# Kernel optimization log

Hardware: AMD Instinct MI355X
Metric: run time of the kernel (lower is better)

Reference implementation:

```python
import jax, jax.numpy as jnp
import numpy as np

EPS = 1e-5  # torch LayerNorm default


def _ln(x, g, b):
    m = jnp.mean(x, axis=-1, keepdims=True)
    v = jnp.mean((x - m) ** 2, axis=-1, keepdims=True)
    return (x - m) / jnp.sqrt(v + EPS) * g + b


def setup_inputs() -> dict:
    key = jax.random.key(0)
    ks = jax.random.split(key, 16)
    B, C, H, S, FF, BINS = 2048, 20, 256, 64, 512, 128
    f32 = jnp.float32
    def w(k, shape, s=0.02):
        return jax.random.normal(k, shape, f32) * s
    return {
        "bitplanes": jax.random.normal(ks[0], (B, C, 8, 8), f32),
        "conv1_w": w(ks[1], (H, C, 3, 3), 0.05), "conv1_b": jnp.zeros((H,), f32),
        "conv2_w": w(ks[2], (H, H, 3, 3), 0.05), "conv2_b": jnp.zeros((H,), f32),
        "in_proj_w": w(ks[3], (3 * H, H)), "in_proj_b": jnp.zeros((3 * H,), f32),
        "out_proj_w": w(ks[4], (H, H)), "out_proj_b": jnp.zeros((H,), f32),
        "ln1_g": jnp.ones((H,), f32), "ln1_b": jnp.zeros((H,), f32),
        "ff1_w": w(ks[5], (FF, H)), "ff1_b": jnp.zeros((FF,), f32),
        "ff2_w": w(ks[6], (H, FF)), "ff2_b": jnp.zeros((H,), f32),
        "ln2_g": jnp.ones((H,), f32), "ln2_b": jnp.zeros((H,), f32),
        "be1_w": w(ks[7], (H, H * S)), "be1_b": jnp.zeros((H,), f32),
        "be2_w": w(ks[8], (H, H)), "be2_b": jnp.zeros((H,), f32),
        "L1_w": w(ks[9], (H, 3 * H)), "L1_b": jnp.zeros((H,), f32),
        "L2_w": w(ks[10], (H, H)), "L2_b": jnp.zeros((H,), f32),
        "Lln_g": jnp.ones((H,), f32), "Lln_b": jnp.zeros((H,), f32),
        "H1_w": w(ks[11], (H, 2 * H)), "H1_b": jnp.zeros((H,), f32),
        "H2_w": w(ks[12], (H, H)), "H2_b": jnp.zeros((H,), f32),
        "Hln_g": jnp.ones((H,), f32), "Hln_b": jnp.zeros((H,), f32),
        "v1_w": w(ks[13], (H, H)), "v1_b": jnp.zeros((H,), f32),
        "v2_w": w(ks[14], (BINS, H)), "v2_b": jnp.zeros((BINS,), f32),
    }


def reference(bitplanes, conv1_w, conv1_b, conv2_w, conv2_b,
              in_proj_w, in_proj_b, out_proj_w, out_proj_b,
              ln1_g, ln1_b, ff1_w, ff1_b, ff2_w, ff2_b, ln2_g, ln2_b,
              be1_w, be1_b, be2_w, be2_b,
              L1_w, L1_b, L2_w, L2_b, Lln_g, Lln_b,
              H1_w, H1_b, H2_w, H2_b, Hln_g, Hln_b,
              v1_w, v1_b, v2_w, v2_b):
    N, T, Hd, nh = 8, 8, 256, 4
    B = bitplanes.shape[0]
    dn = ('NCHW', 'OIHW', 'NCHW')
    # conv encoder on 8x8 board
    x = jax.nn.relu(jax.lax.conv_general_dilated(bitplanes, conv1_w, (1, 1), 'SAME', dimension_numbers=dn) + conv1_b[None, :, None, None])
    x = jax.nn.relu(jax.lax.conv_general_dilated(x, conv2_w, (1, 1), 'SAME', dimension_numbers=dn) + conv2_b[None, :, None, None])
    x = x.reshape(B, Hd, 64).transpose(0, 2, 1)  # [B, 64, 256]
    # TransformerEncoderLayer (post-norm, eval mode => dropout off)
    qkv = x @ in_proj_w.T + in_proj_b  # [B, 64, 768]
    q, k, v = jnp.split(qkv, 3, axis=-1)
    dh = Hd // nh
    heads = lambda t: t.reshape(B, 64, nh, dh).transpose(0, 2, 1, 3)
    q, k, v = heads(q), heads(k), heads(v)
    scale = 1.0 / float(dh) ** 0.5
    a = jax.nn.softmax(jnp.einsum('bhqd,bhkd->bhqk', q, k) * scale, axis=-1)
    o = jnp.einsum('bhqk,bhkd->bhqd', a, v).transpose(0, 2, 1, 3).reshape(B, 64, Hd)
    o = o @ out_proj_w.T + out_proj_b
    x = _ln(x + o, ln1_g, ln1_b)
    ff = jax.nn.relu(x @ ff1_w.T + ff1_b) @ ff2_w.T + ff2_b
    x = _ln(x + ff, ln2_g, ln2_b)
    xf = x.reshape(B, 64 * Hd)  # [B, 16384]
    be = jax.nn.relu(jax.nn.relu(xf @ be1_w.T + be1_b) @ be2_w.T + be2_b)

    def Lnet(zL, zH):
        h = jax.nn.relu(jnp.concatenate([zL, zH, be], axis=-1) @ L1_w.T + L1_b)
        return _ln(jax.nn.relu(h @ L2_w.T + L2_b), Lln_g, Lln_b)

    def Hnet(zH, zL):
        h = jax.nn.relu(jnp.concatenate([zH, zL], axis=-1) @ H1_w.T + H1_b)
        return _ln(jax.nn.relu(h @ H2_w.T + H2_b), Hln_g, Hln_b)

    z0 = jnp.zeros((B, Hd), x.dtype)

    def step(carry, i):
        zH, zL = carry
        zL = Lnet(zL, zH)
        zH = jnp.where((i + 1) % T == 0, Hnet(zH, zL), zH)  # H update every T steps
        return (zH, zL), None

    (zH, zL), _ = jax.lax.scan(step, (z0, z0), jnp.arange(N * T - 1))
    zL = Lnet(zL, zH)
    zH = Hnet(zH, zL)
    return jax.nn.relu(zH @ v1_w.T + v1_b) @ v2_w.T + v2_b  # [B, 128]
```

## Files before the change

kernel.cpp:

```cpp
#include <hip/hip_runtime.h>
#include <hip/hip_bf16.h>
#include <math.h>

#define DEV __device__ __forceinline__

typedef __attribute__((ext_vector_type(8))) short s16x8;
typedef __attribute__((ext_vector_type(4))) float f32x4;

DEV f32x4 MF(s16x8 a, s16x8 b, f32x4 c) {
    return __builtin_amdgcn_mfma_f32_16x16x32_bf16(a, b, c, 0, 0, 0);
}

DEV void split8store(const float v[8], unsigned short* d) {
    s16x8 vh, vm, vl;
#pragma unroll
    for (int j = 0; j < 8; ++j) {
        const float x = v[j];
        const unsigned u = __float_as_uint(x);
        vh[j] = (short)(u >> 16);
        const float r1 = x - __uint_as_float(u & 0xffff0000u);
        const unsigned u1 = __float_as_uint(r1);
        vm[j] = (short)(u1 >> 16);
        const float r2 = r1 - __uint_as_float(u1 & 0xffff0000u);
        vl[j] = (short)(__float_as_uint(r2) >> 16);
    }
    *(s16x8*)(d) = vh;
    *(s16x8*)(d + 512) = vm;
    *(s16x8*)(d + 1024) = vl;
}

__global__ void k_tpose(const float* __restrict__ in, float* __restrict__ out, int N, int K) {
    int total = N * K;
    for (int idx = blockIdx.x * blockDim.x + threadIdx.x; idx < total; idx += gridDim.x * blockDim.x) {
        int n = idx / K, k = idx - n * K;
        out[k * N + n] = in[idx];
    }
}

__global__ void k_wpack(const float* __restrict__ W, unsigned short* __restrict__ WP, int K) {
    const int idx = blockIdx.x * 256 + threadIdx.x;
    const int total = (K >> 5) * 16 * 64;
    if (idx >= total) return;
    const int lane = idx & 63;
    const int nt = (idx >> 6) & 15;
    const int ks = idx >> 10;
    const int col = nt * 16 + (lane & 15);
    const int k0 = ks * 32 + ((lane >> 4) << 3);
    const float* src = W + (size_t)col * K + k0;
    const float4 p = *(const float4*)src;
    const float4 q = *(const float4*)(src + 4);
    const float v[8] = {p.x, p.y, p.z, p.w, q.x, q.y, q.z, q.w};
    split8store(v, WP + (size_t)((ks * 16 + nt) * 3) * 512 + lane * 8);
}

__global__ __launch_bounds__(256) void k_conv1(const float* __restrict__ in, const float* __restrict__ w,
                                               const float* __restrict__ bias, float* __restrict__ out) {
    __shared__ __align__(16) float img[20 * 100];
    const int b = blockIdx.x;
    const int t = threadIdx.x;
    for (int idx = t; idx < 2000; idx += 256) {
        int c = idx / 100, pp = idx - c * 100;
        int y = pp / 10, x = pp - y * 10;
        float v = 0.f;
        if (y >= 1 && y <= 8 && x >= 1 && x <= 8)
            v = in[((size_t)b * 20 + c) * 64 + (y - 1) * 8 + (x - 1)];
        img[idx] = v;
    }
    __syncthreads();
    const int oc = t;
    float acc[64];
    const float bz = bias[oc];
#pragma unroll
    for (int p = 0; p < 64; ++p) acc[p] = bz;
    const float* wrow = w + oc * 180;
    for (int c = 0; c < 20; ++c) {
#pragma unroll
        for (int k = 0; k < 9; ++k) {
            const int ky = k / 3, kx = k - ky * 3;
            const float wv = wrow[c * 9 + k];
            const int base = c * 100 + ky * 10 + kx;
#pragma unroll
            for (int p = 0; p < 64; ++p)
                acc[p] = fmaf(wv, img[base + p + ((p >> 3) << 1)], acc[p]);
        }
    }
    float* orow = out + ((size_t)b * 256 + oc) * 64;
#pragma unroll
    for (int p = 0; p < 64; ++p) orow[p] = fmaxf(acc[p], 0.f);
}

__global__ __launch_bounds__(256) void k_conv2(const float* __restrict__ a1, const float* __restrict__ w2t,
                                               const float* __restrict__ bias, float* __restrict__ xout) {
    __shared__ __align__(16) float img[128 * 100];
    const int b = blockIdx.x;
    const int t = threadIdx.x;
    const int oc0 = (t & 63) * 4;
    const int pg = t >> 6;
    const int pos0 = pg * 16;
    float acc[4][16];
#pragma unroll
    for (int i = 0; i < 4; ++i) {
        const float bz = bias[oc0 + i];
#pragma unroll
        for (int j = 0; j < 16; ++j) acc[i][j] = bz;
    }
    for (int half = 0; half < 2; ++half) {
        __syncthreads();
        for (int idx = t; idx < 12800; idx += 256) {
            int c = idx / 100, pp = idx - c * 100;
            int y = pp / 10, x = pp - y * 10;
            float v = 0.f;
            if (y >= 1 && y <= 8 && x >= 1 && x <= 8)
                v = a1[((size_t)b * 256 + half * 128 + c) * 64 + (y - 1) * 8 + (x - 1)];
            img[idx] = v;
        }
        __syncthreads();
        for (int ic = 0; ic < 128; ++ic) {
            const float* wbase = w2t + (size_t)((half * 128 + ic) * 9) * 256 + oc0;
#pragma unroll
            for (int k = 0; k < 9; ++k) {
                const int ky = k / 3, kx = k - ky * 3;
                const float4 w4 = *(const float4*)(wbase + k * 256);
                const int rb = ic * 100 + ky * 10 + kx + pg * 20;
#pragma unroll
                for (int j = 0; j < 16; ++j) {
                    const float v = img[rb + j + ((j >> 3) << 1)];
                    acc[0][j] = fmaf(v, w4.x, acc[0][j]);
                    acc[1][j] = fmaf(v, w4.y, acc[1][j]);
                    acc[2][j] = fmaf(v, w4.z, acc[2][j]);
                    acc[3][j] = fmaf(v, w4.w, acc[3][j]);
                }
            }
        }
    }
#pragma unroll
    for (int j = 0; j < 16; ++j) {
        float4 o4 = make_float4(fmaxf(acc[0][j], 0.f), fmaxf(acc[1][j], 0.f),
                                fmaxf(acc[2][j], 0.f), fmaxf(acc[3][j], 0.f));
        *(float4*)(xout + ((size_t)b * 64 + pos0 + j) * 256 + oc0) = o4;
    }
}

__global__ __launch_bounds__(512) void k_attn(const float* __restrict__ x, const float* __restrict__ wqkvT,
                                              const float* __restrict__ bqkv, float* __restrict__ o) {
    __shared__ __align__(16) float qs[64 * 65];
    __shared__ __align__(16) float ks[64 * 68];
    __shared__ __align__(16) float vs[64 * 68];
    __shared__ float pmax[8 * 64];
    __shared__ float psum[8 * 64];
    const int b = blockIdx.x, h = blockIdx.y;
    const int t = threadIdx.x;
    const int d = t & 63;
    const int pg = t >> 6;
    float aq[8], ak[8], av[8];
#pragma unroll
    for (int j = 0; j < 8; ++j) { aq[j] = 0.f; ak[j] = 0.f; av[j] = 0.f; }
    const float* xrow = x + ((size_t)b * 64 + pg * 8) * 256;
    const int colq = h * 64 + d;
    for (int kk = 0; kk < 256; kk += 4) {
        float wq[4], wk[4], wv[4];
#pragma unroll
        for (int i = 0; i < 4; ++i) {
            const float* wr = wqkvT + (size_t)(kk + i) * 768;
            wq[i] = wr[colq]; wk[i] = wr[256 + colq]; wv[i] = wr[512 + colq];
        }
#pragma unroll
        for (int j = 0; j < 8; ++j) {
            const float4 xv = *(const float4*)(xrow + j * 256 + kk);
            aq[j] = fmaf(xv.x, wq[0], aq[j]); aq[j] = fmaf(xv.y, wq[1], aq[j]);
            aq[j] = fmaf(xv.z, wq[2], aq[j]); aq[j] = fmaf(xv.w, wq[3], aq[j]);
            ak[j] = fmaf(xv.x, wk[0], ak[j]); ak[j] = fmaf(xv.y, wk[1], ak[j]);
            ak[j] = fmaf(xv.z, wk[2], ak[j]); ak[j] = fmaf(xv.w, wk[3], ak[j]);
            av[j] = fmaf(xv.x, wv[0], av[j]); av[j] = fmaf(xv.y, wv[1], av[j]);
            av[j] = fmaf(xv.z, wv[2], av[j]); av[j] = fmaf(xv.w, wv[3], av[j]);
        }
    }
    const float bq = bqkv[colq], bk = bqkv[256 + colq], bv = bqkv[512 + colq];
#pragma unroll
    for (int j = 0; j < 8; ++j) {
        const int p = pg * 8 + j;
        qs[p * 65 + d] = aq[j] + bq;
        ks[p * 68 + d] = ak[j] + bk;
        vs[p * 68 + d] = av[j] + bv;
    }
    __syncthreads();
    const int r = t & 63;
    const int cg = t >> 6;
    float sc[8];
#pragma unroll
    for (int j = 0; j < 8; ++j) sc[j] = 0.f;
    for (int kk = 0; kk < 64; kk += 4) {
        float qv[4];
#pragma unroll
        for (int i = 0; i < 4; ++i) qv[i] = qs[r * 65 + kk + i];
#pragma unroll
        for (int j = 0; j < 8; ++j) {
            const float4 kv = *(const float4*)(ks + (cg * 8 + j) * 68 + kk);
            sc[j] = fmaf(qv[0], kv.x, sc[j]); sc[j] = fmaf(qv[1], kv.y, sc[j]);
            sc[j] = fmaf(qv[2], kv.z, sc[j]); sc[j] = fmaf(qv[3], kv.w, sc[j]);
        }
    }
    float pm = -1e30f;
#pragma unroll
    for (int j = 0; j < 8; ++j) { sc[j] *= 0.125f; pm = fmaxf(pm, sc[j]); }
    pmax[cg * 64 + r] = pm;
    __syncthreads();
    float m = pmax[r];
#pragma unroll
    for (int i = 1; i < 8; ++i) m = fmaxf(m, pmax[i * 64 + r]);
    float pe[8], ps = 0.f;
#pragma unroll
    for (int j = 0; j < 8; ++j) { pe[j] = __expf(sc[j] - m); ps += pe[j]; }
    psum[cg * 64 + r] = ps;
    __syncthreads();
    float den = psum[r];
#pragma unroll
    for (int i = 1; i < 8; ++i) den += psum[i * 64 + r];
    const float rden = 1.f / den;
#pragma unroll
    for (int j = 0; j < 8; ++j) qs[r * 65 + cg * 8 + j] = pe[j] * rden;
    __syncthreads();
    float oa[8];
#pragma unroll
    for (int j = 0; j < 8; ++j) oa[j] = 0.f;
    for (int c = 0; c < 64; ++c) {
        const float pv = qs[r * 65 + c];
        const float4 v0 = *(const float4*)(vs + c * 68 + cg * 8);
        const float4 v1 = *(const float4*)(vs + c * 68 + cg * 8 + 4);
        oa[0] = fmaf(pv, v0.x, oa[0]); oa[1] = fmaf(pv, v0.y, oa[1]);
        oa[2] = fmaf(pv, v0.z, oa[2]); oa[3] = fmaf(pv, v0.w, oa[3]);
        oa[4] = fmaf(pv, v1.x, oa[4]); oa[5] = fmaf(pv, v1.y, oa[5]);
        oa[6] = fmaf(pv, v1.z, oa[6]); oa[7] = fmaf(pv, v1.w, oa[7]);
    }
#pragma unroll
    for (int j = 0; j < 8; ++j) ks[r * 68 + cg * 8 + j] = oa[j];
    __syncthreads();
    for (int idx = t; idx < 4096; idx += 512) {
        const int rr = idx >> 6, dd = idx & 63;
        o[((size_t)b * 64 + rr) * 256 + h * 64 + dd] = ks[rr * 68 + dd];
    }
}

__global__ __launch_bounds__(256) void k_gemm(const float* __restrict__ A, const float* __restrict__ W,
                                              const float* __restrict__ bias, float* __restrict__ C,
                                              int M, int N, int K, int kChunk, int relu) {
    __shared__ __align__(16) float As[16 * 68];
    __shared__ __align__(16) float Bs[16 * 68];
    const int t = threadIdx.x;
    const int row0 = blockIdx.x * 64;
    const int col0 = blockIdx.y * 64;
    const int k0 = blockIdx.z * kChunk;
    const int k1 = k0 + kChunk;
    float* Cb = C + (size_t)blockIdx.z * M * N;
    const int tr = t >> 4, tc = t & 15;
    const int lr = t >> 2, lc = t & 3;
    float acc[4][4] = {};
    const float* Ap = A + (size_t)(row0 + lr) * K + lc * 4;
    const float* Wp = W + (size_t)(col0 + lr) * K + lc * 4;
    for (int kt = k0; kt < k1; kt += 16) {
        const float4 a4 = *(const float4*)(Ap + kt);
        const float4 w4 = *(const float4*)(Wp + kt);
        As[(lc * 4 + 0) * 68 + lr] = a4.x;
        As[(lc * 4 + 1) * 68 + lr] = a4.y;
        As[(lc * 4 + 2) * 68 + lr] = a4.z;
        As[(lc * 4 + 3) * 68 + lr] = a4.w;
        Bs[(lc * 4 + 0) * 68 + lr] = w4.x;
        Bs[(lc * 4 + 1) * 68 + lr] = w4.y;
        Bs[(lc * 4 + 2) * 68 + lr] = w4.z;
        Bs[(lc * 4 + 3) * 68 + lr] = w4.w;
        __syncthreads();
#pragma unroll
        for (int kk = 0; kk < 16; ++kk) {
            const float4 av = *(const float4*)(As + kk * 68 + tr * 4);
            const float4 bv = *(const float4*)(Bs + kk * 68 + tc * 4);
            acc[0][0] = fmaf(av.x, bv.x, acc[0][0]); acc[0][1] = fmaf(av.x, bv.y, acc[0][1]);
            acc[0][2] = fmaf(av.x, bv.z, acc[0][2]); acc[0][3] = fmaf(av.x, bv.w, acc[0][3]);
            acc[1][0] = fmaf(av.y, bv.x, acc[1][0]); acc[1][1] = fmaf(av.y, bv.y, acc[1][1]);
            acc[1][2] = fmaf(av.y, bv.z, acc[1][2]); acc[1][3] = fmaf(av.y, bv.w, acc[1][3]);
            acc[2][0] = fmaf(av.z, bv.x, acc[2][0]); acc[2][1] = fmaf(av.z, bv.y, acc[2][1]);
            acc[2][2] = fmaf(av.z, bv.z, acc[2][2]); acc[2][3] = fmaf(av.z, bv.w, acc[2][3]);
            acc[3][0] = fmaf(av.w, bv.x, acc[3][0]); acc[3][1] = fmaf(av.w, bv.y, acc[3][1]);
            acc[3][2] = fmaf(av.w, bv.z, acc[3][2]); acc[3][3] = fmaf(av.w, bv.w, acc[3][3]);
        }
        __syncthreads();
    }
    float4 bb = make_float4(0.f, 0.f, 0.f, 0.f);
    if (bias) bb = *(const float4*)(bias + col0 + tc * 4);
#pragma unroll
    for (int i = 0; i < 4; ++i) {
        float4 ov = make_float4(acc[i][0] + bb.x, acc[i][1] + bb.y, acc[i][2] + bb.z, acc[i][3] + bb.w);
        if (relu) {
            ov.x = fmaxf(ov.x, 0.f); ov.y = fmaxf(ov.y, 0.f);
            ov.z = fmaxf(ov.z, 0.f); ov.w = fmaxf(ov.w, 0.f);
        }
        *(float4*)(Cb + (size_t)(row0 + tr * 4 + i) * N + col0 + tc * 4) = ov;
    }
}

__global__ __launch_bounds__(256) void k_ln_add(float* __restrict__ x, const float* __restrict__ add,
                                                const float* __restrict__ g, const float* __restrict__ bta) {
    const int t = threadIdx.x;
    const size_t r = (size_t)blockIdx.x * 4 + (t >> 6);
    const int lane = t & 63;
    float4 xv = *(const float4*)(x + r * 256 + lane * 4);
    const float4 av = *(const float4*)(add + r * 256 + lane * 4);
    const float4 v = make_float4(xv.x + av.x, xv.y + av.y, xv.z + av.z, xv.w + av.w);
    float s = v.x + v.y + v.z + v.w;
    float ss = fmaf(v.x, v.x, fmaf(v.y, v.y, fmaf(v.z, v.z, v.w * v.w)));
#pragma unroll
    for (int m = 32; m; m >>= 1) { s += __shfl_xor(s, m); ss += __shfl_xor(ss, m); }
    const float mean = s * (1.f / 256.f);
    const float var = ss * (1.f / 256.f) - mean * mean;
    const float rstd = rsqrtf(var + 1e-5f);
    const float4 g4 = *(const float4*)(g + lane * 4);
    const float4 b4 = *(const float4*)(bta + lane * 4);
    float4 ov;
    ov.x = (v.x - mean) * rstd * g4.x + b4.x;
    ov.y = (v.y - mean) * rstd * g4.y + b4.y;
    ov.z = (v.z - mean) * rstd * g4.z + b4.z;
    ov.w = (v.w - mean) * rstd * g4.w + b4.w;
    *(float4*)(x + r * 256 + lane * 4) = ov;
}

__global__ void k_be1_reduce(const float* __restrict__ parts, const float* __restrict__ bias,
                             float* __restrict__ out, int n) {
    const int idx = blockIdx.x * blockDim.x + threadIdx.x;
    if (idx < n) {
        float s = bias[idx & 255];
#pragma unroll
        for (int p = 0; p < 8; ++p) s += parts[(size_t)p * n + idx];
        out[idx] = fmaxf(s, 0.f);
    }
}


DEV void splitpass(const float* scr, unsigned short* frag, int t) {
    const int ks = t >> 6, ln = t & 63;
    const int row = ln & 15;
    const int k0 = ks * 32 + ((ln >> 4) << 3);
    const float* s = scr + row * 260 + k0;
    const float4 p = *(const float4*)s;
    const float4 q = *(const float4*)(s + 4);
    const float v[8] = {p.x, p.y, p.z, p.w, q.x, q.y, q.z, q.w};
    split8store(v, frag + (ks * 3) * 512 + ln * 8);
}

DEV void mfma6(f32x4& acc, s16x8 ah, s16x8 am, s16x8 al, const unsigned short* bp) {
    const s16x8 bh = *(const s16x8*)(bp);
    const s16x8 bm = *(const s16x8*)(bp + 512);
    const s16x8 bl = *(const s16x8*)(bp + 1024);
    acc = MF(ah, bh, acc);
    acc = MF(ah, bm, acc);
    acc = MF(am, bh, acc);
    acc = MF(ah, bl, acc);
    acc = MF(al, bh, acc);
    acc = MF(am, bm, acc);
}

DEV void rungemm(f32x4& a0, f32x4& a1, const unsigned short* __restrict__ WP, int KS,
                 const unsigned short* f0, const unsigned short* f1, const unsigned short* f2,
                 int wv, int lane) {
    for (int ks = 0; ks < KS; ++ks) {
        const unsigned short* fa = (ks < 8) ? f0 : ((ks < 16) ? f1 : f2);
        const int kl = ks & 7;
        const unsigned short* ap = fa + (kl * 3) * 512 + lane * 8;
        const s16x8 ah = *(const s16x8*)(ap);
        const s16x8 am = *(const s16x8*)(ap + 512);
        const s16x8 al = *(const s16x8*)(ap + 1024);
        const unsigned short* bp = WP + (size_t)((ks * 16 + wv * 2) * 3) * 512 + lane * 8;
        mfma6(a0, ah, am, al, bp);
        mfma6(a1, ah, am, al, bp + 1536);
    }
}

DEV void storeC(f32x4 a0, f32x4 a1, const float* __restrict__ bias, float* scr, int wv, int lane) {
    const int rb = (lane >> 4) * 4;
    const int c0 = wv * 32 + (lane & 15);
    const float bz0 = bias[c0];
    const float bz1 = bias[c0 + 16];
    scr[(rb + 0) * 260 + c0] = fmaxf(a0[0] + bz0, 0.f);
    scr[(rb + 1) * 260 + c0] = fmaxf(a0[1] + bz0, 0.f);
    scr[(rb + 2) * 260 + c0] = fmaxf(a0[2] + bz0, 0.f);
    scr[(rb + 3) * 260 + c0] = fmaxf(a0[3] + bz0, 0.f);
    scr[(rb + 0) * 260 + c0 + 16] = fmaxf(a1[0] + bz1, 0.f);
    scr[(rb + 1) * 260 + c0 + 16] = fmaxf(a1[1] + bz1, 0.f);
    scr[(rb + 2) * 260 + c0 + 16] = fmaxf(a1[2] + bz1, 0.f);
    scr[(rb + 3) * 260 + c0 + 16] = fmaxf(a1[3] + bz1, 0.f);
}

DEV void lnpass(float* scr, const float* __restrict__ g, const float* __restrict__ bb, int t) {
    const int row = 2 * (t >> 6) + ((t & 63) >> 5);
    const int c0 = (t & 31) * 8;
    float* s = scr + row * 260 + c0;
    const float4 x0 = *(const float4*)s;
    const float4 x1 = *(const float4*)(s + 4);
    float sum = x0.x + x0.y + x0.z + x0.w + x1.x + x1.y + x1.z + x1.w;
    float sq = fmaf(x0.x, x0.x, fmaf(x0.y, x0.y, fmaf(x0.z, x0.z, x0.w * x0.w)));
    sq = fmaf(x1.x, x1.x, fmaf(x1.y, x1.y, fmaf(x1.z, x1.z, fmaf(x1.w, x1.w, sq))));
#pragma unroll
    for (int m = 16; m; m >>= 1) { sum += __shfl_xor(sum, m); sq += __shfl_xor(sq, m); }
    const float mean = sum * (1.f / 256.f);
    const float var = sq * (1.f / 256.f) - mean * mean;
    const float rstd = rsqrtf(var + 1e-5f);
    const float4 g0 = *(const float4*)(g + c0);
    const float4 g1 = *(const float4*)(g + c0 + 4);
    const float4 b0 = *(const float4*)(bb + c0);
    const float4 b1 = *(const float4*)(bb + c0 + 4);
    float4 o0, o1;
    o0.x = (x0.x - mean) * rstd * g0.x + b0.x;
    o0.y = (x0.y - mean) * rstd * g0.y + b0.y;
    o0.z = (x0.z - mean) * rstd * g0.z + b0.z;
    o0.w = (x0.w - mean) * rstd * g0.w + b0.w;
    o1.x = (x1.x - mean) * rstd * g1.x + b1.x;
    o1.y = (x1.y - mean) * rstd * g1.y + b1.y;
    o1.z = (x1.z - mean) * rstd * g1.z + b1.z;
    o1.w = (x1.w - mean) * rstd * g1.w + b1.w;
    *(float4*)s = o0;
    *(float4*)(s + 4) = o1;
}

__global__ __launch_bounds__(512, 1) void k_hrm(const float* __restrict__ be,
        const unsigned short* __restrict__ L1P, const float* __restrict__ L1b,
        const unsigned short* __restrict__ L2P, const float* __restrict__ L2b,
        const float* __restrict__ Lg, const float* __restrict__ Lbt,
        const unsigned short* __restrict__ H1P, const float* __restrict__ H1b,
        const unsigned short* __restrict__ H2P, const float* __restrict__ H2b,
        const float* __restrict__ Hg, const float* __restrict__ Hbt,
        const unsigned short* __restrict__ v1P, const float* __restrict__ v1b,
        const float* __restrict__ v2T, const float* __restrict__ v2b,
        float* __restrict__ out) {
    __shared__ __align__(16) unsigned short fzL[12288];
    __shared__ __align__(16) unsigned short fzH[12288];
    __shared__ __align__(16) unsigned short fbe[12288];
    __shared__ __align__(16) unsigned short fh1[12288];
    __shared__ __align__(16) float scr[16 * 260];
    const int t = threadIdx.x;
    const int b0 = blockIdx.x * 16;
    const int wv = t >> 6, lane = t & 63;
    for (int i = t; i < 12288; i += 512) { fzL[i] = 0; fzH[i] = 0; }
    {
        const int ks = t >> 6, ln = t & 63;
        const int row = ln & 15;
        const int k0 = ks * 32 + ((ln >> 4) << 3);
        const float* s = be + (size_t)(b0 + row) * 256 + k0;
        const float4 p = *(const float4*)s;
        const float4 q = *(const float4*)(s + 4);
        const float v[8] = {p.x, p.y, p.z, p.w, q.x, q.y, q.z, q.w};
        split8store(v, fbe + (ks * 3) * 512 + ln * 8);
    }
    __syncthreads();
    const f32x4 zero4 = {0.f, 0.f, 0.f, 0.f};
    for (int it = 0; it < 64; ++it) {
        f32x4 a0 = zero4, a1 = zero4;
        rungemm(a0, a1, L1P, 24, fzL, fzH, fbe, wv, lane);
        storeC(a0, a1, L1b, scr, wv, lane);
        __syncthreads();
        splitpass(scr, fh1, t);
        __syncthreads();
        a0 = zero4; a1 = zero4;
        rungemm(a0, a1, L2P, 8, fh1, fh1, fh1, wv, lane);
        storeC(a0, a1, L2b, scr, wv, lane);
        __syncthreads();
        lnpass(scr, Lg, Lbt, t);
        __syncthreads();
        splitpass(scr, fzL, t);
        __syncthreads();
        if (((it + 1) & 7) == 0) {
            a0 = zero4; a1 = zero4;
            rungemm(a0, a1, H1P, 16, fzH, fzL, fzL, wv, lane);
            storeC(a0, a1, H1b, scr, wv, lane);
            __syncthreads();
            splitpass(scr, fh1, t);
            __syncthreads();
            a0 = zero4; a1 = zero4;
            rungemm(a0, a1, H2P, 8, fh1, fh1, fh1, wv, lane);
            storeC(a0, a1, H2b, scr, wv, lane);
            __syncthreads();
            lnpass(scr, Hg, Hbt, t);
            __syncthreads();
            splitpass(scr, fzH, t);
            __syncthreads();
        }
    }
    f32x4 a0 = zero4, a1 = zero4;
    rungemm(a0, a1, v1P, 8, fzH, fzH, fzH, wv, lane);
    storeC(a0, a1, v1b, scr, wv, lane);
    __syncthreads();
    for (int idx = t; idx < 2048; idx += 512) {
        const int r = idx >> 7, oo = idx & 127;
        float s = v2b[oo];
        for (int kk = 0; kk < 256; kk += 4) {
            const float4 c4 = *(const float4*)(&scr[r * 260 + kk]);
            s = fmaf(c4.x, v2T[(kk + 0) * 128 + oo], s);
            s = fmaf(c4.y, v2T[(kk + 1) * 128 + oo], s);
            s = fmaf(c4.z, v2T[(kk + 2) * 128 + oo], s);
            s = fmaf(c4.w, v2T[(kk + 3) * 128 + oo], s);
        }
        out[(size_t)(b0 + r) * 128 + oo] = s;
    }
}

extern "C" void kernel_launch(void* const* d_in, const int* in_sizes, int n_in,
                              void* d_out, int out_size, void* d_ws, size_t ws_size,
                              hipStream_t stream) {
    const float* bitplanes  = (const float*)d_in[0];
    const float* conv1_w    = (const float*)d_in[1];
    const float* conv1_b    = (const float*)d_in[2];
    const float* conv2_w    = (const float*)d_in[3];
    const float* conv2_b    = (const float*)d_in[4];
    const float* in_proj_w  = (const float*)d_in[5];
    const float* in_proj_b  = (const float*)d_in[6];
    const float* out_proj_w = (const float*)d_in[7];
    const float* out_proj_b = (const float*)d_in[8];
    const float* ln1_g      = (const float*)d_in[9];
    const float* ln1_b      = (const float*)d_in[10];
    const float* ff1_w      = (const float*)d_in[11];
    const float* ff1_b      = (const float*)d_in[12];
    const float* ff2_w      = (const float*)d_in[13];
    const float* ff2_b      = (const float*)d_in[14];
    const float* ln2_g      = (const float*)d_in[15];
    const float* ln2_b      = (const float*)d_in[16];
    const float* be1_w      = (const float*)d_in[17];
    const float* be1_b      = (const float*)d_in[18];
    const float* be2_w      = (const float*)d_in[19];
    const float* be2_b      = (const float*)d_in[20];
    const float* L1_w       = (const float*)d_in[21];
    const float* L1_b       = (const float*)d_in[22];
    const float* L2_w       = (const float*)d_in[23];
    const float* L2_b       = (const float*)d_in[24];
    const float* Lln_g      = (const float*)d_in[25];
    const float* Lln_b      = (const float*)d_in[26];
    const float* H1_w       = (const float*)d_in[27];
    const float* H1_b       = (const float*)d_in[28];
    const float* H2_w       = (const float*)d_in[29];
    const float* H2_b       = (const float*)d_in[30];
    const float* Hln_g      = (const float*)d_in[31];
    const float* Hln_b      = (const float*)d_in[32];
    const float* v1_w       = (const float*)d_in[33];
    const float* v1_b       = (const float*)d_in[34];
    const float* v2_w       = (const float*)d_in[35];
    const float* v2_b       = (const float*)d_in[36];

    const size_t persist = 2654208ull;
    int CB = 64;
    for (int c = 2048; c >= 64; c >>= 1) {
        size_t needBytes = ((size_t)c * 65536ull + persist) * 4ull;
        if (needBytes <= ws_size) { CB = c; break; }
    }
    const int NCH = 2048 / CB;

    float* ws = (float*)d_ws;
    float* a1buf = ws;
    float* xbuf  = a1buf + (size_t)CB * 16384;
    float* tbuf  = xbuf + (size_t)CB * 16384;
    float* wqkvT = tbuf + (size_t)CB * 32768;
    float* w2t   = wqkvT + 196608;
    float* v2T   = w2t + 589824;
    float* L1Pf  = v2T + 32768;
    float* L2Pf  = L1Pf + 294912;
    float* H1Pf  = L2Pf + 98304;
    float* H2Pf  = H1Pf + 196608;
    float* v1Pf  = H2Pf + 98304;
    float* beB   = v1Pf + 98304;
    float* bemid = beB + 524288;
    unsigned short* L1P = (unsigned short*)L1Pf;
    unsigned short* L2P = (unsigned short*)L2Pf;
    unsigned short* H1P = (unsigned short*)H1Pf;
    unsigned short* H2P = (unsigned short*)H2Pf;
    unsigned short* v1P = (unsigned short*)v1Pf;

    k_tpose<<<256, 256, 0, stream>>>(in_proj_w, wqkvT, 768, 256);
    k_tpose<<<512, 256, 0, stream>>>(conv2_w, w2t, 256, 2304);
    k_tpose<<<64, 256, 0, stream>>>(v2_w, v2T, 128, 256);
    k_wpack<<<96, 256, 0, stream>>>(L1_w, L1P, 768);
    k_wpack<<<32, 256, 0, stream>>>(L2_w, L2P, 256);
    k_wpack<<<64, 256, 0, stream>>>(H1_w, H1P, 512);
    k_wpack<<<32, 256, 0, stream>>>(H2_w, H2P, 256);
    k_wpack<<<32, 256, 0, stream>>>(v1_w, v1P, 256);

    for (int ch = 0; ch < NCH; ++ch) {
        const float* bp_c = bitplanes + (size_t)ch * CB * 20 * 64;
        k_conv1<<<CB, 256, 0, stream>>>(bp_c, conv1_w, conv1_b, a1buf);
        k_conv2<<<CB, 256, 0, stream>>>(a1buf, w2t, conv2_b, xbuf);
        k_attn<<<dim3(CB, 4), 512, 0, stream>>>(xbuf, wqkvT, in_proj_b, a1buf);
        k_gemm<<<dim3(CB, 4, 1), 256, 0, stream>>>(a1buf, out_proj_w, out_proj_b, tbuf,
                                                   CB * 64, 256, 256, 256, 0);
        k_ln_add<<<CB * 16, 256, 0, stream>>>(xbuf, tbuf, ln1_g, ln1_b);
        k_gemm<<<dim3(CB, 8, 1), 256, 0, stream>>>(xbuf, ff1_w, ff1_b, tbuf,
                                                   CB * 64, 512, 256, 256, 1);
        k_gemm<<<dim3(CB, 4, 1), 256, 0, stream>>>(tbuf, ff2_w, ff2_b, a1buf,
                                                   CB * 64, 256, 512, 512, 0);
        k_ln_add<<<CB * 16, 256, 0, stream>>>(xbuf, a1buf, ln2_g, ln2_b);
        k_gemm<<<dim3(CB / 64, 4, 8), 256, 0, stream>>>(xbuf, be1_w, nullptr, tbuf,
                                                        CB, 256, 16384, 2048, 0);
        k_be1_reduce<<<CB, 256, 0, stream>>>(tbuf, be1_b, bemid + (size_t)ch * CB * 256, CB * 256);
        k_gemm<<<dim3(CB / 64, 4, 1), 256, 0, stream>>>(bemid + (size_t)ch * CB * 256, be2_w, be2_b,
                                                        beB + (size_t)ch * CB * 256, CB, 256, 256, 256, 1);
    }

    k_hrm<<<128, 512, 0, stream>>>(beB, L1P, L1_b, L2P, L2_b, Lln_g, Lln_b,
                                   H1P, H1_b, H2P, H2_b, Hln_g, Hln_b,
                                   v1P, v1_b, v2T, v2_b, (float*)d_out);
}
```

Before: 6.144 ms.

## Move conv2 and dense GEMMs to split-bf16 MFMA with prepacked weights

```diff
diff --git a/kernel.cpp b/kernel.cpp
--- a/kernel.cpp
+++ b/kernel.cpp
@@ -11,18 +11,23 @@
     return __builtin_amdgcn_mfma_f32_16x16x32_bf16(a, b, c, 0, 0, 0);
 }
 
+DEV void split3(float x, unsigned short& h, unsigned short& m, unsigned short& l) {
+    const unsigned u = __float_as_uint(x);
+    h = (unsigned short)(u >> 16);
+    const float r1 = x - __uint_as_float(u & 0xffff0000u);
+    const unsigned u1 = __float_as_uint(r1);
+    m = (unsigned short)(u1 >> 16);
+    const float r2 = r1 - __uint_as_float(u1 & 0xffff0000u);
+    l = (unsigned short)(__float_as_uint(r2) >> 16);
+}
+
 DEV void split8store(const float v[8], unsigned short* d) {
     s16x8 vh, vm, vl;
 #pragma unroll
     for (int j = 0; j < 8; ++j) {
-        const float x = v[j];
-        const unsigned u = __float_as_uint(x);
-        vh[j] = (short)(u >> 16);
-        const float r1 = x - __uint_as_float(u & 0xffff0000u);
-        const unsigned u1 = __float_as_uint(r1);
-        vm[j] = (short)(u1 >> 16);
-        const float r2 = r1 - __uint_as_float(u1 & 0xffff0000u);
-        vl[j] = (short)(__float_as_uint(r2) >> 16);
+        unsigned short h, m, l;
+        split3(v[j], h, m, l);
+        vh[j] = (short)h; vm[j] = (short)m; vl[j] = (short)l;
     }
     *(s16x8*)(d) = vh;
     *(s16x8*)(d + 512) = vm;
@@ -37,25 +42,27 @@
     }
 }
 
-__global__ void k_wpack(const float* __restrict__ W, unsigned short* __restrict__ WP, int K) {
+__global__ void k_wpack3(const float* __restrict__ W, unsigned short* __restrict__ WP,
+                         int K, int NT, int ldw, int stride, int off) {
     const int idx = blockIdx.x * 256 + threadIdx.x;
-    const int total = (K >> 5) * 16 * 64;
+    const int total = (K >> 5) * NT * 64;
     if (idx >= total) return;
     const int lane = idx & 63;
-    const int nt = (idx >> 6) & 15;
-    const int ks = idx >> 10;
+    const int nt = (idx >> 6) % NT;
+    const int ks = idx / (64 * NT);
     const int col = nt * 16 + (lane & 15);
     const int k0 = ks * 32 + ((lane >> 4) << 3);
-    const float* src = W + (size_t)col * K + k0;
-    const float4 p = *(const float4*)src;
-    const float4 q = *(const float4*)(src + 4);
-    const float v[8] = {p.x, p.y, p.z, p.w, q.x, q.y, q.z, q.w};
-    split8store(v, WP + (size_t)((ks * 16 + nt) * 3) * 512 + lane * 8);
+    const float* src = W + (size_t)col * ldw + (size_t)k0 * stride + off;
+    float v[8];
+#pragma unroll
+    for (int j = 0; j < 8; ++j) v[j] = src[j * stride];
+    split8store(v, WP + (size_t)((ks * NT + nt) * 3) * 512 + lane * 8);
 }
 
 __global__ __launch_bounds__(256) void k_conv1(const float* __restrict__ in, const float* __restrict__ w,
                                                const float* __restrict__ bias, float* __restrict__ out) {
     __shared__ __align__(16) float img[20 * 100];
+    __shared__ __align__(16) float stg[16 * 260];
     const int b = blockIdx.x;
     const int t = threadIdx.x;
     for (int idx = t; idx < 2000; idx += 256) {
@@ -84,65 +91,93 @@
                 acc[p] = fmaf(wv, img[base + p + ((p >> 3) << 1)], acc[p]);
         }
     }
-    float* orow = out + ((size_t)b * 256 + oc) * 64;
-#pragma unroll
-    for (int p = 0; p < 64; ++p) orow[p] = fmaxf(acc[p], 0.f);
-}
-
-__global__ __launch_bounds__(256) void k_conv2(const float* __restrict__ a1, const float* __restrict__ w2t,
-                                               const float* __restrict__ bias, float* __restrict__ xout) {
-    __shared__ __align__(16) float img[128 * 100];
-    const int b = blockIdx.x;
-    const int t = threadIdx.x;
-    const int oc0 = (t & 63) * 4;
-    const int pg = t >> 6;
-    const int pos0 = pg * 16;
-    float acc[4][16];
-#pragma unroll
-    for (int i = 0; i < 4; ++i) {
-        const float bz = bias[oc0 + i];
-#pragma unroll
-        for (int j = 0; j < 16; ++j) acc[i][j] = bz;
-    }
-    for (int half = 0; half < 2; ++half) {
+#pragma unroll
+    for (int cc = 0; cc < 4; ++cc) {
+        __syncthreads();
+#pragma unroll
+        for (int p = 0; p < 16; ++p) stg[p * 260 + t] = acc[cc * 16 + p];
+        __syncthreads();
+        for (int idx = t; idx < 4096; idx += 256) {
+            const int r = idx >> 8, c = idx & 255;
+            out[((size_t)b * 64 + cc * 16 + r) * 256 + c] = fmaxf(stg[r * 260 + c], 0.f);
+        }
+    }
+}
+
+__global__ __launch_bounds__(256) void k_conv2mf(const float* __restrict__ a1,
+                                                 const unsigned short* __restrict__ WPC2,
+                                                 const float* __restrict__ bias,
+                                                 float* __restrict__ xout) {
+    __shared__ __align__(16) unsigned short AhS[100 * 132];
+    __shared__ __align__(16) unsigned short AmS[100 * 132];
+    __shared__ __align__(16) unsigned short AlS[100 * 132];
+    const int b = blockIdx.x, t = threadIdx.x;
+    const int wv = t >> 6, lane = t & 63;
+    f32x4 acc[16];
+#pragma unroll
+    for (int nt = 0; nt < 16; ++nt) acc[nt] = (f32x4){0.f, 0.f, 0.f, 0.f};
+    const int pl = lane & 15;
+    const int py = pl >> 3, px = pl & 7;
+    const int akoff = (lane >> 4) << 3;
+    for (int h = 0; h < 2; ++h) {
         __syncthreads();
         for (int idx = t; idx < 12800; idx += 256) {
-            int c = idx / 100, pp = idx - c * 100;
-            int y = pp / 10, x = pp - y * 10;
+            const int pr = idx >> 7, c = idx & 127;
+            const int Y = pr / 10, X = pr - Y * 10;
             float v = 0.f;
-            if (y >= 1 && y <= 8 && x >= 1 && x <= 8)
-                v = a1[((size_t)b * 256 + half * 128 + c) * 64 + (y - 1) * 8 + (x - 1)];
-            img[idx] = v;
-        }
-        __syncthreads();
-        for (int ic = 0; ic < 128; ++ic) {
-            const float* wbase = w2t + (size_t)((half * 128 + ic) * 9) * 256 + oc0;
-#pragma unroll
-            for (int k = 0; k < 9; ++k) {
-                const int ky = k / 3, kx = k - ky * 3;
-                const float4 w4 = *(const float4*)(wbase + k * 256);
-                const int rb = ic * 100 + ky * 10 + kx + pg * 20;
-#pragma unroll
-                for (int j = 0; j < 16; ++j) {
-                    const float v = img[rb + j + ((j >> 3) << 1)];
-                    acc[0][j] = fmaf(v, w4.x, acc[0][j]);
-                    acc[1][j] = fmaf(v, w4.y, acc[1][j]);
-                    acc[2][j] = fmaf(v, w4.z, acc[2][j]);
-                    acc[3][j] = fmaf(v, w4.w, acc[3][j]);
+            if (Y >= 1 && Y <= 8 && X >= 1 && X <= 8)
+                v = a1[((size_t)b * 64 + (Y - 1) * 8 + X - 1) * 256 + h * 128 + c];
+            unsigned short hh, mm, ll;
+            split3(v, hh, mm, ll);
+            AhS[pr * 132 + c] = hh;
+            AmS[pr * 132 + c] = mm;
+            AlS[pr * 132 + c] = ll;
+        }
+        __syncthreads();
+#pragma unroll
+        for (int tap = 0; tap < 9; ++tap) {
+            const int dy = tap / 3, dx = tap - dy * 3;
+            const int prow = (wv * 2 + py + dy) * 10 + px + dx;
+            const unsigned short* arh = AhS + prow * 132 + akoff;
+            const unsigned short* arm = AmS + prow * 132 + akoff;
+            const unsigned short* arl = AlS + prow * 132 + akoff;
+#pragma unroll
+            for (int ks = 0; ks < 4; ++ks) {
+                const s16x8 ah = *(const s16x8*)(arh + ks * 32);
+                const s16x8 am = *(const s16x8*)(arm + ks * 32);
+                const s16x8 al = *(const s16x8*)(arl + ks * 32);
+                const unsigned short* bp = WPC2 + (size_t)(tap * 128 + (h * 4 + ks) * 16) * 1536 + lane * 8;
+#pragma unroll
+                for (int nt = 0; nt < 16; ++nt) {
+                    const unsigned short* bb = bp + nt * 1536;
+                    const s16x8 bh = *(const s16x8*)(bb);
+                    const s16x8 bm = *(const s16x8*)(bb + 512);
+                    const s16x8 bl = *(const s16x8*)(bb + 1024);
+                    acc[nt] = MF(ah, bh, acc[nt]);
+                    acc[nt] = MF(ah, bm, acc[nt]);
+                    acc[nt] = MF(am, bh, acc[nt]);
+                    acc[nt] = MF(ah, bl, acc[nt]);
+                    acc[nt] = MF(al, bh, acc[nt]);
+                    acc[nt] = MF(am, bm, acc[nt]);
                 }
             }
         }
     }
-#pragma unroll
-    for (int j = 0; j < 16; ++j) {
-        float4 o4 = make_float4(fmaxf(acc[0][j], 0.f), fmaxf(acc[1][j], 0.f),
-                                fmaxf(acc[2][j], 0.f), fmaxf(acc[3][j], 0.f));
-        *(float4*)(xout + ((size_t)b * 64 + pos0 + j) * 256 + oc0) = o4;
+    const int prow0 = wv * 16 + ((lane >> 4) << 2);
+    const int ccol = lane & 15;
+#pragma unroll
+    for (int nt = 0; nt < 16; ++nt) {
+        const float bz = bias[nt * 16 + ccol];
+#pragma unroll
+        for (int i = 0; i < 4; ++i)
+            xout[((size_t)b * 64 + prow0 + i) * 256 + nt * 16 + ccol] = fmaxf(acc[nt][i] + bz, 0.f);
     }
 }
 
 __global__ __launch_bounds__(512) void k_attn(const float* __restrict__ x, const float* __restrict__ wqkvT,
-                                              const float* __restrict__ bqkv, float* __restrict__ o) {
+                                              const float* __restrict__ bqkv,
+                                              unsigned short* __restrict__ oh, unsigned short* __restrict__ om,
+                                              unsigned short* __restrict__ ol) {
     __shared__ __align__(16) float qs[64 * 65];
     __shared__ __align__(16) float ks[64 * 68];
     __shared__ __align__(16) float vs[64 * 68];
@@ -237,68 +272,98 @@
     __syncthreads();
     for (int idx = t; idx < 4096; idx += 512) {
         const int rr = idx >> 6, dd = idx & 63;
-        o[((size_t)b * 64 + rr) * 256 + h * 64 + dd] = ks[rr * 68 + dd];
-    }
-}
-
-__global__ __launch_bounds__(256) void k_gemm(const float* __restrict__ A, const float* __restrict__ W,
-                                              const float* __restrict__ bias, float* __restrict__ C,
-                                              int M, int N, int K, int kChunk, int relu) {
-    __shared__ __align__(16) float As[16 * 68];
-    __shared__ __align__(16) float Bs[16 * 68];
+        const float v = ks[rr * 68 + dd];
+        unsigned short hh, mm, ll;
+        split3(v, hh, mm, ll);
+        const size_t o = ((size_t)b * 64 + rr) * 256 + h * 64 + dd;
+        oh[o] = hh;
+        om[o] = mm;
+        ol[o] = ll;
+    }
+}
+
+__global__ __launch_bounds__(256) void k_gemm_mf(
+    const unsigned short* __restrict__ Ah, const unsigned short* __restrict__ Am,
+    const unsigned short* __restrict__ Al,
+    const unsigned short* __restrict__ WP, const float* __restrict__ bias,
+    float* __restrict__ Cf, unsigned short* __restrict__ Ch, unsigned short* __restrict__ Cm,
+    unsigned short* __restrict__ Cl,
+    int M, int N, int K, int kChunk, int relu) {
     const int t = threadIdx.x;
-    const int row0 = blockIdx.x * 64;
+    const int wv = t >> 6, lane = t & 63;
+    const int row0 = blockIdx.x * 64 + wv * 16;
     const int col0 = blockIdx.y * 64;
+    const int NT = N >> 4;
     const int k0 = blockIdx.z * kChunk;
-    const int k1 = k0 + kChunk;
-    float* Cb = C + (size_t)blockIdx.z * M * N;
-    const int tr = t >> 4, tc = t & 15;
-    const int lr = t >> 2, lc = t & 3;
-    float acc[4][4] = {};
-    const float* Ap = A + (size_t)(row0 + lr) * K + lc * 4;
-    const float* Wp = W + (size_t)(col0 + lr) * K + lc * 4;
-    for (int kt = k0; kt < k1; kt += 16) {
-        const float4 a4 = *(const float4*)(Ap + kt);
-        const float4 w4 = *(const float4*)(Wp + kt);
-        As[(lc * 4 + 0) * 68 + lr] = a4.x;
-        As[(lc * 4 + 1) * 68 + lr] = a4.y;
-        As[(lc * 4 + 2) * 68 + lr] = a4.z;
-        As[(lc * 4 + 3) * 68 + lr] = a4.w;
-        Bs[(lc * 4 + 0) * 68 + lr] = w4.x;
-        Bs[(lc * 4 + 1) * 68 + lr] = w4.y;
-        Bs[(lc * 4 + 2) * 68 + lr] = w4.z;
-        Bs[(lc * 4 + 3) * 68 + lr] = w4.w;
-        __syncthreads();
-#pragma unroll
-        for (int kk = 0; kk < 16; ++kk) {
-            const float4 av = *(const float4*)(As + kk * 68 + tr * 4);
-            const float4 bv = *(const float4*)(Bs + kk * 68 + tc * 4);
-            acc[0][0] = fmaf(av.x, bv.x, acc[0][0]); acc[0][1] = fmaf(av.x, bv.y, acc[0][1]);
-            acc[0][2] = fmaf(av.x, bv.z, acc[0][2]); acc[0][3] = fmaf(av.x, bv.w, acc[0][3]);
-            acc[1][0] = fmaf(av.y, bv.x, acc[1][0]); acc[1][1] = fmaf(av.y, bv.y, acc[1][1]);
-            acc[1][2] = fmaf(av.y, bv.z, acc[1][2]); acc[1][3] = fmaf(av.y, bv.w, acc[1][3]);
-            acc[2][0] = fmaf(av.z, bv.x, acc[2][0]); acc[2][1] = fmaf(av.z, bv.y, acc[2][1]);
-            acc[2][2] = fmaf(av.z, bv.z, acc[2][2]); acc[2][3] = fmaf(av.z, bv.w, acc[2][3]);
-            acc[3][0] = fmaf(av.w, bv.x, acc[3][0]); acc[3][1] = fmaf(av.w, bv.y, acc[3][1]);
-            acc[3][2] = fmaf(av.w, bv.z, acc[3][2]); acc[3][3] = fmaf(av.w, bv.w, acc[3][3]);
-        }
-        __syncthreads();
-    }
-    float4 bb = make_float4(0.f, 0.f, 0.f, 0.f);
-    if (bias) bb = *(const float4*)(bias + col0 + tc * 4);
-#pragma unroll
-    for (int i = 0; i < 4; ++i) {
-        float4 ov = make_float4(acc[i][0] + bb.x, acc[i][1] + bb.y, acc[i][2] + bb.z, acc[i][3] + bb.w);
-        if (relu) {
-            ov.x = fmaxf(ov.x, 0.f); ov.y = fmaxf(ov.y, 0.f);
-            ov.z = fmaxf(ov.z, 0.f); ov.w = fmaxf(ov.w, 0.f);
-        }
-        *(float4*)(Cb + (size_t)(row0 + tr * 4 + i) * N + col0 + tc * 4) = ov;
+    const int nks = kChunk >> 5;
+    f32x4 acc[4];
+#pragma unroll
+    for (int nt = 0; nt < 4; ++nt) acc[nt] = (f32x4){0.f, 0.f, 0.f, 0.f};
+    const int arow = row0 + (lane & 15);
+    const size_t aoff = (size_t)arow * K + k0 + ((lane >> 4) << 3);
+    const unsigned short* aph = Ah + aoff;
+    const unsigned short* apm = Am + aoff;
+    const unsigned short* apl = Al + aoff;
+    const unsigned short* bp = WP + ((size_t)((k0 >> 5) * NT + (col0 >> 4))) * 1536 + lane * 8;
+    const size_t bstride = (size_t)NT * 1536;
+    for (int ks = 0; ks < nks; ++ks) {
+        const s16x8 ah = *(const s16x8*)aph;
+        const s16x8 am = *(const s16x8*)apm;
+        const s16x8 al = *(const s16x8*)apl;
+        aph += 32; apm += 32; apl += 32;
+#pragma unroll
+        for (int nt = 0; nt < 4; ++nt) {
+            const unsigned short* bb = bp + nt * 1536;
+            const s16x8 bh = *(const s16x8*)(bb);
+            const s16x8 bm = *(const s16x8*)(bb + 512);
+            const s16x8 bl = *(const s16x8*)(bb + 1024);
+            acc[nt] = MF(ah, bh, acc[nt]);
+            acc[nt] = MF(ah, bm, acc[nt]);
+            acc[nt] = MF(am, bh, acc[nt]);
+            acc[nt] = MF(ah, bl, acc[nt]);
+            acc[nt] = MF(al, bh, acc[nt]);
+            acc[nt] = MF(am, bm, acc[nt]);
+        }
+        bp += bstride;
+    }
+    const int crow = row0 + ((lane >> 4) << 2);
+    const int ccol = col0 + (lane & 15);
+    float bz[4];
+#pragma unroll
+    for (int nt = 0; nt < 4; ++nt) bz[nt] = bias ? bias[ccol + nt * 16] : 0.f;
+    if (Ch) {
+#pragma unroll
+        for (int nt = 0; nt < 4; ++nt) {
+#pragma unroll
+            for (int i = 0; i < 4; ++i) {
+                float v = acc[nt][i] + bz[nt];
+                if (relu) v = fmaxf(v, 0.f);
+                unsigned short hh, mm, ll;
+                split3(v, hh, mm, ll);
+                const size_t o = (size_t)(crow + i) * N + ccol + nt * 16;
+                Ch[o] = hh;
+                Cm[o] = mm;
+                Cl[o] = ll;
+            }
+        }
+    } else {
+        float* base = Cf + (size_t)blockIdx.z * M * N;
+#pragma unroll
+        for (int nt = 0; nt < 4; ++nt) {
+#pragma unroll
+            for (int i = 0; i < 4; ++i) {
+                float v = acc[nt][i] + bz[nt];
+                if (relu) v = fmaxf(v, 0.f);
+                base[(size_t)(crow + i) * N + ccol + nt * 16] = v;
+            }
+        }
     }
 }
 
 __global__ __launch_bounds__(256) void k_ln_add(float* __restrict__ x, const float* __restrict__ add,
-                                                const float* __restrict__ g, const float* __restrict__ bta) {
+                                                const float* __restrict__ g, const float* __restrict__ bta,
+                                                unsigned short* __restrict__ sh, unsigned short* __restrict__ sm,
+                                                unsigned short* __restrict__ sl) {
     const int t = threadIdx.x;
     const size_t r = (size_t)blockIdx.x * 4 + (t >> 6);
     const int lane = t & 63;
@@ -320,19 +385,31 @@
     ov.z = (v.z - mean) * rstd * g4.z + b4.z;
     ov.w = (v.w - mean) * rstd * g4.w + b4.w;
     *(float4*)(x + r * 256 + lane * 4) = ov;
+    const float vv[4] = {ov.x, ov.y, ov.z, ov.w};
+    unsigned short hh[4], mm[4], ll[4];
+#pragma unroll
+    for (int j = 0; j < 4; ++j) split3(vv[j], hh[j], mm[j], ll[j]);
+    *(ushort4*)(sh + r * 256 + lane * 4) = make_ushort4(hh[0], hh[1], hh[2], hh[3]);
+    *(ushort4*)(sm + r * 256 + lane * 4) = make_ushort4(mm[0], mm[1], mm[2], mm[3]);
+    *(ushort4*)(sl + r * 256 + lane * 4) = make_ushort4(ll[0], ll[1], ll[2], ll[3]);
 }
 
 __global__ void k_be1_reduce(const float* __restrict__ parts, const float* __restrict__ bias,
-                             float* __restrict__ out, int n) {
+                             unsigned short* __restrict__ oh, unsigned short* __restrict__ om,
+                             unsigned short* __restrict__ ol, int n) {
     const int idx = blockIdx.x * blockDim.x + threadIdx.x;
     if (idx < n) {
         float s = bias[idx & 255];
 #pragma unroll
         for (int p = 0; p < 8; ++p) s += parts[(size_t)p * n + idx];
-        out[idx] = fmaxf(s, 0.f);
-    }
-}
-
+        s = fmaxf(s, 0.f);
+        unsigned short hh, mm, ll;
+        split3(s, hh, mm, ll);
+        oh[idx] = hh;
+        om[idx] = mm;
+        ol[idx] = ll;
+    }
+}
 
 DEV void splitpass(const float* scr, unsigned short* frag, int t) {
     const int ks = t >> 6, ln = t & 63;
@@ -541,10 +618,10 @@
     const float* v2_w       = (const float*)d_in[35];
     const float* v2_b       = (const float*)d_in[36];
 
-    const size_t persist = 2654208ull;
+    const size_t persist = 9306112ull;
     int CB = 64;
     for (int c = 2048; c >= 64; c >>= 1) {
-        size_t needBytes = ((size_t)c * 65536ull + persist) * 4ull;
+        size_t needBytes = ((size_t)c * 106880ull + persist) * 4ull;
         if (needBytes <= ws_size) { CB = c; break; }
     }
     const int NCH = 2048 / CB;
@@ -552,50 +629,83 @@
     float* ws = (float*)d_ws;
     float* a1buf = ws;
     float* xbuf  = a1buf + (size_t)CB * 16384;
-    float* tbuf  = xbuf + (size_t)CB * 16384;
-    float* wqkvT = tbuf + (size_t)CB * 32768;
-    float* w2t   = wqkvT + 196608;
-    float* v2T   = w2t + 589824;
+    float* sbuf  = xbuf + (size_t)CB * 16384;
+    float* tbuf  = sbuf + (size_t)CB * 24576;
+    float* bemf  = tbuf + (size_t)CB * 49152;
+    float* wqkvT = bemf + (size_t)CB * 384;
+    float* v2T   = wqkvT + 196608;
     float* L1Pf  = v2T + 32768;
     float* L2Pf  = L1Pf + 294912;
     float* H1Pf  = L2Pf + 98304;
     float* H2Pf  = H1Pf + 196608;
     float* v1Pf  = H2Pf + 98304;
     float* beB   = v1Pf + 98304;
-    float* bemid = beB + 524288;
+    float* wpOf  = beB + 524288;
+    float* wpF1f = wpOf + 98304;
+    float* wpF2f = wpF1f + 196608;
+    float* wpB1f = wpF2f + 196608;
+    float* wpB2f = wpB1f + 6291456;
+    float* wpC2f = wpB2f + 98304;
+
+    unsigned short* soh = (unsigned short*)sbuf;
+    unsigned short* som = soh + (size_t)CB * 16384;
+    unsigned short* sol = som + (size_t)CB * 16384;
+    unsigned short* tbh = (unsigned short*)tbuf;
+    unsigned short* tbm = tbh + (size_t)CB * 32768;
+    unsigned short* tbl = tbm + (size_t)CB * 32768;
+    unsigned short* bemh = (unsigned short*)bemf;
+    unsigned short* bemm = bemh + (size_t)CB * 256;
+    unsigned short* beml = bemm + (size_t)CB * 256;
     unsigned short* L1P = (unsigned short*)L1Pf;
     unsigned short* L2P = (unsigned short*)L2Pf;
     unsigned short* H1P = (unsigned short*)H1Pf;
     unsigned short* H2P = (unsigned short*)H2Pf;
     unsigned short* v1P = (unsigned short*)v1Pf;
+    unsigned short* wpO = (unsigned short*)wpOf;
+    unsigned short* wpF1 = (unsigned short*)wpF1f;
+    unsigned short* wpF2 = (unsigned short*)wpF2f;
+    unsigned short* wpB1 = (unsigned short*)wpB1f;
+    unsigned short* wpB2 = (unsigned short*)wpB2f;
+    unsigned short* wpC2 = (unsigned short*)wpC2f;
 
     k_tpose<<<256, 256, 0, stream>>>(in_proj_w, wqkvT, 768, 256);
-    k_tpose<<<512, 256, 0, stream>>>(conv2_w, w2t, 256, 2304);
     k_tpose<<<64, 256, 0, stream>>>(v2_w, v2T, 128, 256);
-    k_wpack<<<96, 256, 0, stream>>>(L1_w, L1P, 768);
-    k_wpack<<<32, 256, 0, stream>>>(L2_w, L2P, 256);
-    k_wpack<<<64, 256, 0, stream>>>(H1_w, H1P, 512);
-    k_wpack<<<32, 256, 0, stream>>>(H2_w, H2P, 256);
-    k_wpack<<<32, 256, 0, stream>>>(v1_w, v1P, 256);
+    k_wpack3<<<96, 256, 0, stream>>>(L1_w, L1P, 768, 16, 768, 1, 0);
+    k_wpack3<<<32, 256, 0, stream>>>(L2_w, L2P, 256, 16, 256, 1, 0);
+    k_wpack3<<<64, 256, 0, stream>>>(H1_w, H1P, 512, 16, 512, 1, 0);
+    k_wpack3<<<32, 256, 0, stream>>>(H2_w, H2P, 256, 16, 256, 1, 0);
+    k_wpack3<<<32, 256, 0, stream>>>(v1_w, v1P, 256, 16, 256, 1, 0);
+    k_wpack3<<<32, 256, 0, stream>>>(out_proj_w, wpO, 256, 16, 256, 1, 0);
+    k_wpack3<<<64, 256, 0, stream>>>(ff1_w, wpF1, 256, 32, 256, 1, 0);
+    k_wpack3<<<64, 256, 0, stream>>>(ff2_w, wpF2, 512, 16, 512, 1, 0);
+    k_wpack3<<<2048, 256, 0, stream>>>(be1_w, wpB1, 16384, 16, 16384, 1, 0);
+    k_wpack3<<<32, 256, 0, stream>>>(be2_w, wpB2, 256, 16, 256, 1, 0);
+    for (int tap = 0; tap < 9; ++tap)
+        k_wpack3<<<32, 256, 0, stream>>>(conv2_w, wpC2 + (size_t)tap * 196608, 256, 16, 2304, 9, tap);
 
     for (int ch = 0; ch < NCH; ++ch) {
         const float* bp_c = bitplanes + (size_t)ch * CB * 20 * 64;
         k_conv1<<<CB, 256, 0, stream>>>(bp_c, conv1_w, conv1_b, a1buf);
-        k_conv2<<<CB, 256, 0, stream>>>(a1buf, w2t, conv2_b, xbuf);
-        k_attn<<<dim3(CB, 4), 512, 0, stream>>>(xbuf, wqkvT, in_proj_b, a1buf);
-        k_gemm<<<dim3(CB, 4, 1), 256, 0, stream>>>(a1buf, out_proj_w, out_proj_b, tbuf,
-                                                   CB * 64, 256, 256, 256, 0);
-        k_ln_add<<<CB * 16, 256, 0, stream>>>(xbuf, tbuf, ln1_g, ln1_b);
-        k_gemm<<<dim3(CB, 8, 1), 256, 0, stream>>>(xbuf, ff1_w, ff1_b, tbuf,
-                                                   CB * 64, 512, 256, 256, 1);
-        k_gemm<<<dim3(CB, 4, 1), 256, 0, stream>>>(tbuf, ff2_w, ff2_b, a1buf,
-                                                   CB * 64, 256, 512, 512, 0);
-        k_ln_add<<<CB * 16, 256, 0, stream>>>(xbuf, a1buf, ln2_g, ln2_b);
-        k_gemm<<<dim3(CB / 64, 4, 8), 256, 0, stream>>>(xbuf, be1_w, nullptr, tbuf,
-                                                        CB, 256, 16384, 2048, 0);
-        k_be1_reduce<<<CB, 256, 0, stream>>>(tbuf, be1_b, bemid + (size_t)ch * CB * 256, CB * 256);
-        k_gemm<<<dim3(CB / 64, 4, 1), 256, 0, stream>>>(bemid + (size_t)ch * CB * 256, be2_w, be2_b,
-                                                        beB + (size_t)ch * CB * 256, CB, 256, 256, 256, 1);
+        k_conv2mf<<<CB, 256, 0, stream>>>(a1buf, wpC2, conv2_b, xbuf);
+        k_attn<<<dim3(CB, 4), 512, 0, stream>>>(xbuf, wqkvT, in_proj_b, soh, som, sol);
+        k_gemm_mf<<<dim3(CB, 4, 1), 256, 0, stream>>>(soh, som, sol, wpO, out_proj_b,
+                                                      tbuf, nullptr, nullptr, nullptr,
+                                                      CB * 64, 256, 256, 256, 0);
+        k_ln_add<<<CB * 16, 256, 0, stream>>>(xbuf, tbuf, ln1_g, ln1_b, soh, som, sol);
+        k_gemm_mf<<<dim3(CB, 8, 1), 256, 0, stream>>>(soh, som, sol, wpF1, ff1_b,
+                                                      nullptr, tbh, tbm, tbl,
+                                                      CB * 64, 512, 256, 256, 1);
+        k_gemm_mf<<<dim3(CB, 4, 1), 256, 0, stream>>>(tbh, tbm, tbl, wpF2, ff2_b,
+                                                      a1buf, nullptr, nullptr, nullptr,
+                                                      CB * 64, 256, 512, 512, 0);
+        k_ln_add<<<CB * 16, 256, 0, stream>>>(xbuf, a1buf, ln2_g, ln2_b, soh, som, sol);
+        k_gemm_mf<<<dim3(CB / 64, 4, 8), 256, 0, stream>>>(soh, som, sol, wpB1, nullptr,
+                                                           tbuf, nullptr, nullptr, nullptr,
+                                                           CB, 256, 16384, 2048, 0);
+        k_be1_reduce<<<CB, 256, 0, stream>>>(tbuf, be1_b, bemh, bemm, beml, CB * 256);
+        k_gemm_mf<<<dim3(CB / 64, 4, 1), 256, 0, stream>>>(bemh, bemm, beml, wpB2, be2_b,
+                                                           beB + (size_t)ch * CB * 256, nullptr, nullptr, nullptr,
+                                                           CB, 256, 256, 256, 1);
     }
 
     k_hrm<<<128, 512, 0, stream>>>(beB, L1P, L1_b, L2P, L2_b, Lln_g, Lln_b,
```

Result: faster. 5.957 ms (-3.0%).
